# Performance work log

Measured on AMD Instinct MI355X. Metric: run time of the kernel, lower is better.

## Reference

```python
import jax, jax.numpy as jnp
import numpy as np

B, N, D, L = 32, 1000, 256, 3


def setup_inputs() -> dict:
    key = jax.random.key(0)
    k1, k2, k3, k4 = jax.random.split(key, 4)
    x = jax.random.normal(k1, (B, N, D), dtype=jnp.float32)
    node_feature = jax.random.normal(k2, (B, N, D), dtype=jnp.float32)
    # GCNConv weights (PyG Linear, glorot) and biases, stacked over layers
    scale = jnp.sqrt(6.0 / (D + D)).astype(jnp.float32)
    Ws = jax.random.uniform(k3, (L, D, D), minval=-1.0, maxval=1.0, dtype=jnp.float32) * scale
    bs = jnp.zeros((L, D), dtype=jnp.float32)
    return {"x": x, "node_feature": node_feature, "Ws": Ws, "bs": bs}


def _gcn_norm_adj(n):
    # self_loop=False -> adjacency is all-ones (diagonal included), so
    # add_remaining_self_loops is a no-op; deg = n for every node.
    adj = jnp.ones((n, n), dtype=jnp.float32)
    deg = adj.sum(axis=1)
    dinv = jax.lax.rsqrt(deg)
    return dinv[:, None] * adj * dinv[None, :]  # == ones/n


def reference(x, node_feature, Ws, bs):
    # x is unused by the math (only its size is inspected in the original).
    A_norm = _gcn_norm_adj(node_feature.shape[1])
    h = node_feature
    for l in range(L):
        h = jnp.einsum('bnd,de->bne', h, Ws[l])          # linear transform
        h = jnp.einsum('mn,bnd->bmd', A_norm, h) + bs[l]  # normalized aggregation + bias
        if l < L - 1:
            h = jax.nn.relu(h)  # dropout is identity in eval mode
    update_node_feature = h + node_feature  # residual (unconditional in source)
    return (update_node_feature, node_feature)
```

## Files before the change

### kernel.cpp

```cpp
#include <hip/hip_runtime.h>

#define BB 32
#define NN 1000
#define DD 256
#define SS 25
#define RPS 40
#define ELEMS (BB * NN * DD)
#define WF4 (3 * DD * DD / 4)

typedef float f4 __attribute__((ext_vector_type(4)));

__global__ __launch_bounds__(256) void k_sumcopy(const f4* __restrict__ nf4,
                                                 f4* __restrict__ out1_4,
                                                 float* __restrict__ partials,
                                                 const f4* __restrict__ W4) {
    const int s = blockIdx.x, b = blockIdx.y, t = threadIdx.x;
    const int r4 = t >> 6, c = t & 63;
    f4 acc = (f4)(0.f);
#pragma unroll
    for (int i = 0; i < RPS / 4; i++) {
        const int n = s * RPS + i * 4 + r4;
        const int idx = (b * NN + n) * (DD / 4) + c;
        f4 v = nf4[idx];
        out1_4[idx] = v;
        acc += v;
    }
    {
        const int bid = b * SS + s;
#pragma unroll
        for (int i = 0; i < 2; i++) {
            const int idx = (bid * 512 + i * 256 + t) % WF4;
            f4 w = W4[idx];
            asm volatile("" :: "v"(w.x), "v"(w.y), "v"(w.z), "v"(w.w));
        }
    }
    __shared__ float red[1024];
    ((f4*)red)[r4 * 64 + c] = acc;
    __syncthreads();
    partials[(b * SS + s) * DD + t] =
        red[t] + red[256 + t] + red[512 + t] + red[768 + t];
}

__global__ __launch_bounds__(256) void k_mlp(const float* __restrict__ partials,
                                             const float* __restrict__ Ws,
                                             const float* __restrict__ bsv,
                                             float* __restrict__ hrow) {
    const int b = blockIdx.x, t = threadIdx.x;
    __shared__ float h[2][DD];

    float a0 = 0.f, a1 = 0.f, a2 = 0.f, a3 = 0.f;
#pragma unroll
    for (int sp = 0; sp < 24; sp += 4) {
        a0 += partials[(b * SS + sp + 0) * DD + t];
        a1 += partials[(b * SS + sp + 1) * DD + t];
        a2 += partials[(b * SS + sp + 2) * DD + t];
        a3 += partials[(b * SS + sp + 3) * DD + t];
    }
    a0 += partials[(b * SS + 24) * DD + t];
    h[0][t] = ((a0 + a1) + (a2 + a3)) * (1.0f / (float)NN);
    __syncthreads();

    int cur = 0;
    for (int l = 0; l < 3; l++) {
        const float* __restrict__ W = Ws + l * DD * DD;
        float c0 = 0.f, c1 = 0.f, c2 = 0.f, c3 = 0.f;
#pragma unroll 8
        for (int k4 = 0; k4 < DD / 4; k4++) {
            const float* Wk = W + (k4 * 4) * DD + t;
            c0 = fmaf(h[cur][k4 * 4 + 0], Wk[0 * DD], c0);
            c1 = fmaf(h[cur][k4 * 4 + 1], Wk[1 * DD], c1);
            c2 = fmaf(h[cur][k4 * 4 + 2], Wk[2 * DD], c2);
            c3 = fmaf(h[cur][k4 * 4 + 3], Wk[3 * DD], c3);
        }
        float a = ((c0 + c1) + (c2 + c3)) + bsv[l * DD + t];
        if (l < 2) {
            h[cur ^ 1][t] = fmaxf(a, 0.f);
            cur ^= 1;
            __syncthreads();
        } else {
            hrow[b * DD + t] = a;
        }
    }
}

__global__ __launch_bounds__(256) void k_out0(const f4* __restrict__ nf4,
                                              const float* __restrict__ hrow,
                                              f4* __restrict__ out0_4) {
    const int i = blockIdx.x * 256 + threadIdx.x;
    const int e = i * 4;
    const int b = e / (NN * DD);
    const int d0 = e & (DD - 1);
    f4 v = nf4[i];
    const f4 hv = *(const f4*)(hrow + b * DD + d0);
    out0_4[i] = v + hv;
}

extern "C" void kernel_launch(void* const* d_in, const int* in_sizes, int n_in,
                              void* d_out, int out_size, void* d_ws, size_t ws_size,
                              hipStream_t stream) {
    const f4* nf4    = (const f4*)d_in[1];
    const float* Ws  = (const float*)d_in[2];
    const float* bsv = (const float*)d_in[3];
    f4* out0 = (f4*)d_out;
    f4* out1 = (f4*)((float*)d_out + ELEMS);

    float* partials = (float*)d_ws;
    float* hrow     = partials + SS * BB * DD;

    k_sumcopy<<<dim3(SS, BB), 256, 0, stream>>>(nf4, out1, partials, (const f4*)Ws);
    k_mlp<<<BB, 256, 0, stream>>>(partials, Ws, bsv, hrow);
    k_out0<<<(ELEMS / 4) / 256, 256, 0, stream>>>(nf4, hrow, out0);
}
```

Measured before the change: 134.3 us.

## Fuse MLP into output kernel with redundant per-slice compute and nontemporal stores

Merges the small per-batch MLP kernel and the broadcast-add output kernel into one launch. Each of 10 slices per batch recomputes the three 256x256 matvecs in shared memory, then writes its share of node_feature plus h. Stores to both outputs now use nontemporal hints. This removes one kernel launch and the hrow round trip through global memory. In exchange it repeats the MLP work tenfold and runs only 320 blocks for the output phase, which may limit memory parallelism.

```diff
diff --git a/kernel.cpp b/kernel.cpp
--- a/kernel.cpp
+++ b/kernel.cpp
@@ -5,6 +5,8 @@
 #define DD 256
 #define SS 25
 #define RPS 40
+#define OS 10
+#define OF4 (NN * DD / 4 / OS)
 #define ELEMS (BB * NN * DD)
 #define WF4 (3 * DD * DD / 4)
 
@@ -22,7 +24,7 @@
         const int n = s * RPS + i * 4 + r4;
         const int idx = (b * NN + n) * (DD / 4) + c;
         f4 v = nf4[idx];
-        out1_4[idx] = v;
+        __builtin_nontemporal_store(v, &out1_4[idx]);
         acc += v;
     }
     {
@@ -41,12 +43,14 @@
         red[t] + red[256 + t] + red[512 + t] + red[768 + t];
 }
 
-__global__ __launch_bounds__(256) void k_mlp(const float* __restrict__ partials,
-                                             const float* __restrict__ Ws,
-                                             const float* __restrict__ bsv,
-                                             float* __restrict__ hrow) {
-    const int b = blockIdx.x, t = threadIdx.x;
+__global__ __launch_bounds__(256) void k_mlp_out0(const f4* __restrict__ nf4,
+                                                  const float* __restrict__ partials,
+                                                  const float* __restrict__ Ws,
+                                                  const float* __restrict__ bsv,
+                                                  f4* __restrict__ out0_4) {
+    const int s = blockIdx.x, b = blockIdx.y, t = threadIdx.x;
     __shared__ float h[2][DD];
+    __shared__ float hfin[DD];
 
     float a0 = 0.f, a1 = 0.f, a2 = 0.f, a3 = 0.f;
 #pragma unroll
@@ -78,21 +82,18 @@
             cur ^= 1;
             __syncthreads();
         } else {
-            hrow[b * DD + t] = a;
+            hfin[t] = a;
+            __syncthreads();
         }
     }
-}
 
-__global__ __launch_bounds__(256) void k_out0(const f4* __restrict__ nf4,
-                                              const float* __restrict__ hrow,
-                                              f4* __restrict__ out0_4) {
-    const int i = blockIdx.x * 256 + threadIdx.x;
-    const int e = i * 4;
-    const int b = e / (NN * DD);
-    const int d0 = e & (DD - 1);
-    f4 v = nf4[i];
-    const f4 hv = *(const f4*)(hrow + b * DD + d0);
-    out0_4[i] = v + hv;
+    const f4 hv = ((const f4*)hfin)[t & 63];
+    const int base = b * (NN * DD / 4) + s * OF4 + t;
+#pragma unroll
+    for (int i = 0; i < OF4 / 256; i++) {
+        f4 v = nf4[base + i * 256];
+        __builtin_nontemporal_store(v + hv, &out0_4[base + i * 256]);
+    }
 }
 
 extern "C" void kernel_launch(void* const* d_in, const int* in_sizes, int n_in,
@@ -105,9 +106,7 @@
     f4* out1 = (f4*)((float*)d_out + ELEMS);
 
     float* partials = (float*)d_ws;
-    float* hrow     = partials + SS * BB * DD;
 
     k_sumcopy<<<dim3(SS, BB), 256, 0, stream>>>(nf4, out1, partials, (const f4*)Ws);
-    k_mlp<<<BB, 256, 0, stream>>>(partials, Ws, bsv, hrow);
-    k_out0<<<(ELEMS / 4) / 256, 256, 0, stream>>>(nf4, hrow, out0);
+    k_mlp_out0<<<dim3(OS, BB), 256, 0, stream>>>(nf4, partials, Ws, bsv, out0);
 }
```

Result: faster. 131.0 us (-2.5%).
